# Kernel optimization log

Measured on AMD Instinct MI355X. Metric: run time of the kernel, lower is better.

## Reference

```python
import jax, jax.numpy as jnp
import numpy as np

B, C, T, COLS = 256, 1, 128, 512
IN_DIM = C * COLS          # 512
EMB = 1024
HID = 1024
NUM_LAYERS = 2
NUM_CLASSES = 10


def setup_inputs() -> dict:
    key = jax.random.key(0)
    ks = jax.random.split(key, 16)
    s = 0.05
    inp = {
        "x": jax.random.normal(ks[0], (B, C, T, COLS), dtype=jnp.float32),
        "W_enc": jax.random.normal(ks[1], (EMB, IN_DIM), dtype=jnp.float32) * s,
        "b_enc": jnp.zeros((EMB,), dtype=jnp.float32),
        # layer 0: input size EMB
        "W_ih0": jax.random.normal(ks[2], (4 * HID, EMB), dtype=jnp.float32) * s,
        "W_hh0": jax.random.normal(ks[3], (4 * HID, HID), dtype=jnp.float32) * s,
        "b_ih0": jnp.zeros((4 * HID,), dtype=jnp.float32),
        "b_hh0": jnp.zeros((4 * HID,), dtype=jnp.float32),
        # layer 1: input size HID
        "W_ih1": jax.random.normal(ks[4], (4 * HID, HID), dtype=jnp.float32) * s,
        "W_hh1": jax.random.normal(ks[5], (4 * HID, HID), dtype=jnp.float32) * s,
        "b_ih1": jnp.zeros((4 * HID,), dtype=jnp.float32),
        "b_hh1": jnp.zeros((4 * HID,), dtype=jnp.float32),
        "W_cls": jax.random.normal(ks[6], (NUM_CLASSES, HID), dtype=jnp.float32) * s,
        "b_cls": jnp.zeros((NUM_CLASSES,), dtype=jnp.float32),
    }
    return inp


def _lstm_cell(x, h, c, W_ih, W_hh, b_ih, b_hh):
    # gates: [B, 4H], PyTorch gate order i, f, g, o
    gates = x @ W_ih.T + b_ih + h @ W_hh.T + b_hh
    i, f, g, o = jnp.split(gates, 4, axis=-1)
    i = jax.nn.sigmoid(i)
    f = jax.nn.sigmoid(f)
    g = jnp.tanh(g)
    o = jax.nn.sigmoid(o)
    c_new = f * c + i * g
    h_new = o * jnp.tanh(c_new)
    return h_new, c_new


def reference(x, W_enc, b_enc, W_ih0, W_hh0, b_ih0, b_hh0,
              W_ih1, W_hh1, b_ih1, b_hh1, W_cls, b_cls):
    b_size = x.shape[0]
    # [B, C, T, COLS] -> [B, T, C*COLS]
    x_rowed = x.reshape(b_size, T, IN_DIM)
    emb = x_rowed @ W_enc.T + b_enc            # [B, T, EMB]
    emb_t = jnp.transpose(emb, (1, 0, 2))      # [T, B, EMB]

    layer_params = [(W_ih0, W_hh0, b_ih0, b_hh0), (W_ih1, W_hh1, b_ih1, b_hh1)]
    h0 = jnp.zeros((NUM_LAYERS, b_size, HID), dtype=x.dtype)
    c0 = jnp.zeros((NUM_LAYERS, b_size, HID), dtype=x.dtype)

    def step(carry, x_t):
        h, c = carry  # each [L, B, H]
        inp = x_t
        hs, cs = [], []
        for l in range(NUM_LAYERS):
            h_l, c_l = _lstm_cell(inp, h[l], c[l], *layer_params[l])
            hs.append(h_l)
            cs.append(c_l)
            inp = h_l
        return (jnp.stack(hs), jnp.stack(cs)), inp

    (_, _), outs = jax.lax.scan(step, (h0, c0), emb_t)  # outs: [T, B, H]
    last = outs[-1]                                     # [B, H]
    y = last @ W_cls.T + b_cls                          # [B, 10]
    return y
```

## Files before the change

### kernel.cpp

```cpp
#include <hip/hip_runtime.h>

#define B_SZ   256
#define T_SZ   128
#define IN_DIM 512
#define EMB    1024
#define HID    1024
#define G4     4096
#define NCLS   10
#define PSTR   2560
#define NBLK   256

typedef __attribute__((ext_vector_type(8))) short short8v;
typedef __attribute__((ext_vector_type(4))) float floatx4;

__device__ __forceinline__ unsigned short bf16hi(float f) {
    union { float f; unsigned u; } v; v.f = f;
    unsigned r = v.u + 0x7fff + ((v.u >> 16) & 1);
    return (unsigned short)(r >> 16);
}
__device__ __forceinline__ float bf2f(unsigned short b) {
    union { unsigned u; float f; } v; v.u = ((unsigned)b) << 16;
    return v.f;
}

template<int BM,int BN,int BK,int TM,int TN>
__global__ __launch_bounds__((BM/TM)*(BN/TN))
void gemm_f32_nn(const float* __restrict__ A, const float* __restrict__ Bm,
                 float* __restrict__ C, int M, int N, int K) {
    constexpr int THREADS = (BM/TM)*(BN/TN);
    __shared__ float As[BK][BM+4];
    __shared__ float Bs[BK][BN+4];
    const int tid  = threadIdx.x;
    const int tcol = tid % (BN/TN);
    const int trow = tid / (BN/TN);
    const int bm   = blockIdx.y * BM;
    const int bn   = blockIdx.x * BN;
    float acc[TM][TN];
#pragma unroll
    for (int i = 0; i < TM; ++i)
#pragma unroll
        for (int j = 0; j < TN; ++j) acc[i][j] = 0.f;
    for (int k0 = 0; k0 < K; k0 += BK) {
#pragma unroll
        for (int r = 0; r < BM*BK/4; r += THREADS) {
            int i  = r + tid;
            int m  = i / (BK/4);
            int kk = (i % (BK/4)) * 4;
            const float4 v = *(const float4*)(&A[(size_t)(bm+m)*K + k0 + kk]);
            As[kk+0][m]=v.x; As[kk+1][m]=v.y; As[kk+2][m]=v.z; As[kk+3][m]=v.w;
        }
#pragma unroll
        for (int r = 0; r < BK*BN/4; r += THREADS) {
            int i  = r + tid;
            int kk = i / (BN/4);
            int n4 = (i % (BN/4)) * 4;
            const float4 v = *(const float4*)(&Bm[(size_t)(k0+kk)*N + bn + n4]);
            *(float4*)(&Bs[kk][n4]) = v;
        }
        __syncthreads();
#pragma unroll
        for (int k = 0; k < BK; ++k) {
            float a[TM], b[TN];
#pragma unroll
            for (int i = 0; i < TM; ++i) a[i] = As[k][trow*TM+i];
#pragma unroll
            for (int j = 0; j < TN; ++j) b[j] = Bs[k][tcol*TN+j];
#pragma unroll
            for (int i = 0; i < TM; ++i)
#pragma unroll
                for (int j = 0; j < TN; ++j) acc[i][j] += a[i]*b[j];
        }
        __syncthreads();
    }
#pragma unroll
    for (int i = 0; i < TM; ++i)
#pragma unroll
        for (int j = 0; j < TN; ++j)
            C[(size_t)(bm+trow*TM+i)*N + bn + tcol*TN + j] = acc[i][j];
}

__global__ void swz2(const float* __restrict__ M0, int K0, int kf0,
                     const float* __restrict__ M1, int K1, int kfcnt,
                     unsigned short* __restrict__ dst) {
    int gid = blockIdx.x * 256 + threadIdx.x;
    int l   = gid & 63;
    int kf  = (gid >> 6) % kfcnt;
    int cf  = gid / (64 * kfcnt);
    int n   = cf*16 + (l & 15);
    int row = ((n & 3) << 10) + (n >> 2);
    const float* src; int kk = (l >> 4) * 8;
    if (kf < kf0) { src = M0 + (size_t)row * K0; kk += kf * 32; }
    else          { src = M1 + (size_t)row * K1; kk += (kf - kf0) * 32; }
    short8v vh, vl;
#pragma unroll
    for (int j = 0; j < 8; ++j) {
        float f = src[kk + j];
        unsigned short h = bf16hi(f);
        vh[j] = (short)h;
        vl[j] = (short)bf16hi(f - bf2f(h));
    }
    size_t base = ((size_t)(cf * kfcnt + kf) * 2) * 512 + (size_t)l * 8;
    *(short8v*)(dst + base)       = vh;
    *(short8v*)(dst + base + 512) = vl;
}

__global__ void build_bcombI(const float* __restrict__ W_ih0, const float* __restrict__ b_enc,
                             const float* __restrict__ b_ih0, const float* __restrict__ b_hh0,
                             float* __restrict__ bcombI) {
    int row  = blockIdx.x * 4 + (threadIdx.x >> 6);
    int lane = threadIdx.x & 63;
    const float* w = W_ih0 + (size_t)row * EMB;
    float s = 0.f;
    for (int k = lane; k < EMB; k += 64) s += w[k] * b_enc[k];
#pragma unroll
    for (int o = 32; o > 0; o >>= 1) s += __shfl_down(s, o);
    if (lane == 0) {
        int n = ((row & 1023) << 2) | (row >> 10);
        bcombI[n] = s + b_ih0[row] + b_hh0[row];
    }
}

__global__ void addvI(const float* __restrict__ a, const float* __restrict__ b,
                      float* __restrict__ o) {
    int i = blockIdx.x * 256 + threadIdx.x;
    int n = ((i & 1023) << 2) | (i >> 10);
    o[n] = a[i] + b[i];
}

__device__ __forceinline__ void gridbar(unsigned* bar, unsigned target, int tid) {
    __syncthreads();
    if (tid == 0) {
        __threadfence();
        atomicAdd(bar, 1u);
        while (__hip_atomic_load(bar, __ATOMIC_RELAXED, __HIP_MEMORY_SCOPE_AGENT) < target)
            __builtin_amdgcn_s_sleep(1);
        __threadfence();
    }
    __syncthreads();
}

__device__ __forceinline__ void load_b(const unsigned short* bp0, const unsigned short* bp1, int kf,
                                       short8v& h0, short8v& l0, short8v& h1, short8v& l1) {
    const unsigned short* p0 = bp0 + (size_t)kf * 1024;
    const unsigned short* p1 = bp1 + (size_t)kf * 1024;
    h0 = *(const short8v*)p0; l0 = *(const short8v*)(p0 + 512);
    h1 = *(const short8v*)p1; l1 = *(const short8v*)(p1 + 512);
}

__device__ __forceinline__ void mfma24(const unsigned short (*A)[2][64][8], int rowhalf, int l,
                                       short8v bh0, short8v bl0, short8v bh1, short8v bl1,
                                       floatx4 (&acc)[4][2]) {
    short8v ah[4], al[4];
#pragma unroll
    for (int m = 0; m < 4; ++m) {
        ah[m] = *(const short8v*)&A[rowhalf*4 + m][0][l][0];
        al[m] = *(const short8v*)&A[rowhalf*4 + m][1][l][0];
    }
#pragma unroll
    for (int m = 0; m < 4; ++m) {
        acc[m][0] = __builtin_amdgcn_mfma_f32_16x16x32_bf16(ah[m], bh0, acc[m][0], 0, 0, 0);
        acc[m][0] = __builtin_amdgcn_mfma_f32_16x16x32_bf16(ah[m], bl0, acc[m][0], 0, 0, 0);
        acc[m][0] = __builtin_amdgcn_mfma_f32_16x16x32_bf16(al[m], bh0, acc[m][0], 0, 0, 0);
        acc[m][1] = __builtin_amdgcn_mfma_f32_16x16x32_bf16(ah[m], bh1, acc[m][1], 0, 0, 0);
        acc[m][1] = __builtin_amdgcn_mfma_f32_16x16x32_bf16(ah[m], bl1, acc[m][1], 0, 0, 0);
        acc[m][1] = __builtin_amdgcn_mfma_f32_16x16x32_bf16(al[m], bh1, acc[m][1], 0, 0, 0);
    }
}

__device__ __forceinline__ void store_xz(unsigned short* ph, unsigned short* pl,
                                         int bid, int tid, float2 xv) {
    unsigned short h0 = bf16hi(xv.x), h1 = bf16hi(xv.y);
    ushort2 hh; hh.x = h0; hh.y = h1;
    ushort2 lv; lv.x = bf16hi(xv.x - bf2f(h0)); lv.y = bf16hi(xv.y - bf2f(h1));
    size_t o = (size_t)bid * PSTR + tid * 2;
    *(ushort2*)(ph + o) = hh;
    *(ushort2*)(pl + o) = lv;
}

typedef unsigned short AslT[2][8][2][64][8];

__global__ __launch_bounds__(512, 1)
void lstm_persist(const float* __restrict__ x,
                  const unsigned short* __restrict__ WLz,
                  const unsigned short* __restrict__ WRz,
                  const float* __restrict__ biasLI, const float* __restrict__ biasRI,
                  unsigned short* __restrict__ p0h, unsigned short* __restrict__ p0l,
                  unsigned short* __restrict__ p1h, unsigned short* __restrict__ p1l,
                  const float* __restrict__ Wcls, const float* __restrict__ bcls,
                  float* __restrict__ out, unsigned* __restrict__ bar) {
    __shared__ unsigned char smem[65536];
    AslT*  Asl   = (AslT*)smem;
    float (*gtile)[68] = (float (*)[68])smem;

    const int tid = threadIdx.x, bid = blockIdx.x;
    const int w = tid >> 6, l = tid & 63;
    const int kgrp = w >> 2, sub = w & 3;
    const int rowhalf = sub & 1, colhalf = sub >> 1;
    const int cg = bid & 127, rg = bid >> 7;
    const bool is_left = (cg < 64);
    const int cgl = is_left ? cg : cg - 64;
    const int SMAX = is_left ? 24 : 32;
    const int kfcnt = 2 * SMAX;
    const int acol0 = is_left ? 0 : 512;
    const int hcol0 = is_left ? 512 : 1536;
    const int r0 = rg * 128;
    const unsigned short* Bz = is_left ? WLz : WRz;
    const float* biasI = is_left ? biasLI : biasRI;

    const int cf0 = cgl*4 + colhalf*2;
    const unsigned short* bp0 = Bz + ((size_t)cf0     * kfcnt) * 1024 + (size_t)l * 8;
    const unsigned short* bp1 = Bz + ((size_t)(cf0+1) * kfcnt) * 1024 + (size_t)l * 8;
    const int kbase = kgrp * SMAX;

    float bias0 = 0.f, bias1 = 0.f;
    if (kgrp == 0) {
        int cA = cgl*64 + colhalf*32 + (l & 15);
        bias0 = biasI[cA]; bias1 = biasI[cA + 16];
    }

    unsigned short* PH[2] = {p0h, p1h};
    unsigned short* PL[2] = {p0l, p1l};

    float cst[4];
#pragma unroll
    for (int i = 0; i < 4; ++i) cst[i] = 0.f;

    unsigned target = 0;

    if (tid < 256) {
        float2 xv = *(const float2*)&x[((size_t)bid * T_SZ) * IN_DIM + tid * 2];
        store_xz(p0h, p0l, bid, tid, xv);
    }
    target += NBLK; gridbar(bar, target, tid);

    for (int t = 0; t <= T_SZ; ++t) {
        const int cur = t & 1, nxt = cur ^ 1;
        const bool conv = (t < T_SZ - 1) && (tid < 256);
        float2 xv;
        if (conv) xv = *(const float2*)&x[((size_t)bid * T_SZ + t + 1) * IN_DIM + tid * 2];

        const bool active = is_left ? (t < T_SZ) : (t >= 1);
        if (active) {
            const unsigned short* ph  = PH[cur];
            const unsigned short* plo = PL[cur];

            floatx4 acc[4][2];
#pragma unroll
            for (int m = 0; m < 4; ++m) {
                acc[m][0] = (floatx4){bias0, bias0, bias0, bias0};
                acc[m][1] = (floatx4){bias1, bias1, bias1, bias1};
            }

            short8v sreg[4];
            auto stage_load = [&](int s1) {
#pragma unroll
                for (int i = 0; i < 4; ++i) {
                    int seg = w*4 + i;
                    int g = seg >> 4, mf = (seg >> 1) & 7, pl = seg & 1;
                    const unsigned short* p = pl ? plo : ph;
                    size_t o = (size_t)(r0 + mf*16 + (l & 15)) * PSTR
                             + acol0 + (g*SMAX + s1)*32 + ((l >> 4) * 8);
                    sreg[i] = *(const short8v*)(p + o);
                }
            };
            auto stage_write = [&](int b) {
#pragma unroll
                for (int i = 0; i < 4; ++i) {
                    int seg = w*4 + i;
                    int g = seg >> 4, mf = (seg >> 1) & 7, pl = seg & 1;
                    *(short8v*)&Asl[g][b][mf][pl][l][0] = sreg[i];
                }
            };

            short8v bAh0,bAl0,bAh1,bAl1, bBh0,bBl0,bBh1,bBl1;

            stage_load(0); stage_write(0);
            load_b(bp0, bp1, kbase + 0, bAh0, bAl0, bAh1, bAl1);
            load_b(bp0, bp1, kbase + 1, bBh0, bBl0, bBh1, bBl1);
            stage_load(1);
            __syncthreads();

            for (int s2 = 0; s2 < SMAX; s2 += 2) {
                if (s2 + 1 < SMAX) stage_write(1);
                if (s2 + 2 < SMAX) stage_load(s2 + 2);
                mfma24((const unsigned short (*)[2][64][8])Asl[kgrp][0],
                       rowhalf, l, bAh0, bAl0, bAh1, bAl1, acc);
                if (s2 + 2 < SMAX) load_b(bp0, bp1, kbase + s2 + 2, bAh0, bAl0, bAh1, bAl1);
                __syncthreads();
                if (s2 + 2 < SMAX) stage_write(0);
                if (s2 + 3 < SMAX) stage_load(s2 + 3);
                if (s2 + 1 < SMAX)
                    mfma24((const unsigned short (*)[2][64][8])Asl[kgrp][1],
                           rowhalf, l, bBh0, bBl0, bBh1, bBl1, acc);
                if (s2 + 3 < SMAX) load_b(bp0, bp1, kbase + s2 + 3, bBh0, bBl0, bBh1, bBl1);
                __syncthreads();
            }

            if (kgrp == 0) {
#pragma unroll
                for (int m = 0; m < 4; ++m)
#pragma unroll
                    for (int c = 0; c < 2; ++c) {
                        int col = colhalf*32 + c*16 + (l & 15);
#pragma unroll
                        for (int jj = 0; jj < 4; ++jj)
                            gtile[rowhalf*64 + m*16 + ((l >> 4)*4) + jj][col] = acc[m][c][jj];
                    }
            }
            __syncthreads();
            if (kgrp == 1) {
#pragma unroll
                for (int m = 0; m < 4; ++m)
#pragma unroll
                    for (int c = 0; c < 2; ++c) {
                        int col = colhalf*32 + c*16 + (l & 15);
#pragma unroll
                        for (int jj = 0; jj < 4; ++jj)
                            gtile[rowhalf*64 + m*16 + ((l >> 4)*4) + jj][col] += acc[m][c][jj];
                    }
            }
            __syncthreads();

            {
                int u = tid & 15, rq = tid >> 4;
                unsigned short* nh = PH[nxt];
                unsigned short* nl = PL[nxt];
#pragma unroll
                for (int i = 0; i < 4; ++i) {
                    int r = rq*4 + i;
                    float4 gq = *(const float4*)&gtile[r][4*u];
                    float ii = 1.f / (1.f + expf(-gq.x));
                    float ff = 1.f / (1.f + expf(-gq.y));
                    float gg = tanhf(gq.z);
                    float oo = 1.f / (1.f + expf(-gq.w));
                    float cn = ff * cst[i] + ii * gg;
                    cst[i] = cn;
                    float h = oo * tanhf(cn);
                    unsigned short hh = bf16hi(h);
                    size_t o = (size_t)(r0 + r) * PSTR + hcol0 + cgl*16 + u;
                    nh[o] = hh;
                    nl[o] = bf16hi(h - bf2f(hh));
                }
            }
        }

        if (conv) store_xz(PH[nxt], PL[nxt], bid, tid, xv);
        target += NBLK; gridbar(bar, target, tid);
    }

    {
        const unsigned short* hh = PH[(T_SZ + 1) & 1];
        const unsigned short* hl = PL[(T_SZ + 1) & 1];
        float part[NCLS];
#pragma unroll
        for (int n = 0; n < NCLS; ++n) part[n] = 0.f;
        for (int k = tid; k < HID; k += 512) {
            size_t o = (size_t)bid * PSTR + 1536 + k;
            float hv = bf2f(hh[o]) + bf2f(hl[o]);
#pragma unroll
            for (int n = 0; n < NCLS; ++n) part[n] += hv * Wcls[(size_t)n * HID + k];
        }
        float* red = (float*)smem;
        for (int n = 0; n < NCLS; ++n) {
            red[tid] = part[n];
            __syncthreads();
            for (int s = 256; s > 0; s >>= 1) {
                if (tid < s) red[tid] += red[tid + s];
                __syncthreads();
            }
            if (tid == 0) out[(size_t)bid * NCLS + n] = red[0] + bcls[n];
            __syncthreads();
        }
    }
}

extern "C" void kernel_launch(void* const* d_in, const int* in_sizes, int n_in,
                              void* d_out, int out_size, void* d_ws, size_t ws_size,
                              hipStream_t stream) {
    const float* x      = (const float*)d_in[0];
    const float* W_enc  = (const float*)d_in[1];
    const float* b_enc  = (const float*)d_in[2];
    const float* W_ih0  = (const float*)d_in[3];
    const float* W_hh0  = (const float*)d_in[4];
    const float* b_ih0  = (const float*)d_in[5];
    const float* b_hh0  = (const float*)d_in[6];
    const float* W_ih1  = (const float*)d_in[7];
    const float* W_hh1  = (const float*)d_in[8];
    const float* b_ih1  = (const float*)d_in[9];
    const float* b_hh1  = (const float*)d_in[10];
    const float* W_cls  = (const float*)d_in[11];
    const float* b_cls  = (const float*)d_in[12];
    float* out = (float*)d_out;

    float* ws = (float*)d_ws;
    size_t off = 0;
    unsigned short* WLz    = (unsigned short*)(ws + off); off += (size_t)G4 * 1536 * 2 / 2;
    unsigned short* WRz    = (unsigned short*)(ws + off); off += (size_t)G4 * 2048 * 2 / 2;
    float*          Wcomb  = ws + off;                    off += (size_t)G4 * IN_DIM;
    float*          biasLI = ws + off;                    off += G4;
    float*          biasRI = ws + off;                    off += G4;
    unsigned short* planes = (unsigned short*)(ws + off); off += (size_t)4 * B_SZ * PSTR / 2;
    unsigned*       bar    = (unsigned*)(ws + off);       off += 64;

    unsigned short* p0h = planes;
    unsigned short* p0l = p0h + (size_t)B_SZ * PSTR;
    unsigned short* p1h = p0l + (size_t)B_SZ * PSTR;
    unsigned short* p1l = p1h + (size_t)B_SZ * PSTR;

    gemm_f32_nn<128,128,16,8,8><<<dim3(IN_DIM/128, G4/128), 256, 0, stream>>>(
        W_ih0, W_enc, Wcomb, G4, IN_DIM, EMB);
    build_bcombI<<<G4/4, 256, 0, stream>>>(W_ih0, b_enc, b_ih0, b_hh0, biasLI);
    addvI<<<G4/256, 256, 0, stream>>>(b_ih1, b_hh1, biasRI);
    swz2<<<64*48, 256, 0, stream>>>(Wcomb, IN_DIM, 16, W_hh0, HID, 48, WLz);
    swz2<<<64*64, 256, 0, stream>>>(W_ih1, HID, 32, W_hh1, HID, 64, WRz);
    hipMemsetAsync(planes, 0, (size_t)4 * B_SZ * PSTR * 2, stream);
    hipMemsetAsync(bar, 0, sizeof(unsigned), stream);

    lstm_persist<<<NBLK, 512, 0, stream>>>(
        x, WLz, WRz, biasLI, biasRI,
        p0h, p0l, p1h, p1l, W_cls, b_cls, out, bar);
}
```

Before: 8.384 ms.

## Load A fragments directly to registers, drop LDS staging, remap blocks

The per-step GEMM no longer stages A (hidden-state hi/lo) tiles through shared memory with syncthreads between stages. Each wave now loads its A fragments straight from global memory into registers in a double-buffered slice, alongside the B weights. Block-to-(column group, row group) mapping is permuted, and launch bounds allow two blocks per CU with smaller LDS. The aim is to remove LDS round-trips and intra-step barriers, at the cost of redundant global/L2 reads of A across waves and higher register pressure.

New measurement: 11.02 ms. 31.4% more time.

```diff
diff --git a/kernel.cpp b/kernel.cpp
--- a/kernel.cpp
+++ b/kernel.cpp
@@ -139,34 +139,6 @@
     __syncthreads();
 }
 
-__device__ __forceinline__ void load_b(const unsigned short* bp0, const unsigned short* bp1, int kf,
-                                       short8v& h0, short8v& l0, short8v& h1, short8v& l1) {
-    const unsigned short* p0 = bp0 + (size_t)kf * 1024;
-    const unsigned short* p1 = bp1 + (size_t)kf * 1024;
-    h0 = *(const short8v*)p0; l0 = *(const short8v*)(p0 + 512);
-    h1 = *(const short8v*)p1; l1 = *(const short8v*)(p1 + 512);
-}
-
-__device__ __forceinline__ void mfma24(const unsigned short (*A)[2][64][8], int rowhalf, int l,
-                                       short8v bh0, short8v bl0, short8v bh1, short8v bl1,
-                                       floatx4 (&acc)[4][2]) {
-    short8v ah[4], al[4];
-#pragma unroll
-    for (int m = 0; m < 4; ++m) {
-        ah[m] = *(const short8v*)&A[rowhalf*4 + m][0][l][0];
-        al[m] = *(const short8v*)&A[rowhalf*4 + m][1][l][0];
-    }
-#pragma unroll
-    for (int m = 0; m < 4; ++m) {
-        acc[m][0] = __builtin_amdgcn_mfma_f32_16x16x32_bf16(ah[m], bh0, acc[m][0], 0, 0, 0);
-        acc[m][0] = __builtin_amdgcn_mfma_f32_16x16x32_bf16(ah[m], bl0, acc[m][0], 0, 0, 0);
-        acc[m][0] = __builtin_amdgcn_mfma_f32_16x16x32_bf16(al[m], bh0, acc[m][0], 0, 0, 0);
-        acc[m][1] = __builtin_amdgcn_mfma_f32_16x16x32_bf16(ah[m], bh1, acc[m][1], 0, 0, 0);
-        acc[m][1] = __builtin_amdgcn_mfma_f32_16x16x32_bf16(ah[m], bl1, acc[m][1], 0, 0, 0);
-        acc[m][1] = __builtin_amdgcn_mfma_f32_16x16x32_bf16(al[m], bh1, acc[m][1], 0, 0, 0);
-    }
-}
-
 __device__ __forceinline__ void store_xz(unsigned short* ph, unsigned short* pl,
                                          int bid, int tid, float2 xv) {
     unsigned short h0 = bf16hi(xv.x), h1 = bf16hi(xv.y);
@@ -177,9 +149,12 @@
     *(ushort2*)(pl + o) = lv;
 }
 
-typedef unsigned short AslT[2][8][2][64][8];
-
-__global__ __launch_bounds__(512, 1)
+struct SliceRegs {
+    short8v ah[4], al[4];
+    short8v bh0, bl0, bh1, bl1;
+};
+
+__global__ __launch_bounds__(512, 2)
 void lstm_persist(const float* __restrict__ x,
                   const unsigned short* __restrict__ WLz,
                   const unsigned short* __restrict__ WRz,
@@ -188,15 +163,14 @@
                   unsigned short* __restrict__ p1h, unsigned short* __restrict__ p1l,
                   const float* __restrict__ Wcls, const float* __restrict__ bcls,
                   float* __restrict__ out, unsigned* __restrict__ bar) {
-    __shared__ unsigned char smem[65536];
-    AslT*  Asl   = (AslT*)smem;
-    float (*gtile)[68] = (float (*)[68])smem;
+    __shared__ float gtile[128][68];
 
     const int tid = threadIdx.x, bid = blockIdx.x;
     const int w = tid >> 6, l = tid & 63;
     const int kgrp = w >> 2, sub = w & 3;
     const int rowhalf = sub & 1, colhalf = sub >> 1;
-    const int cg = bid & 127, rg = bid >> 7;
+    const int cg = (bid & 7) * 16 + (bid >> 4);
+    const int rg = (bid >> 3) & 1;
     const bool is_left = (cg < 64);
     const int cgl = is_left ? cg : cg - 64;
     const int SMAX = is_left ? 24 : 32;
@@ -212,6 +186,9 @@
     const unsigned short* bp1 = Bz + ((size_t)(cf0+1) * kfcnt) * 1024 + (size_t)l * 8;
     const int kbase = kgrp * SMAX;
 
+    const int arow = r0 + rowhalf*64 + (l & 15);
+    const int akol = (l >> 4) * 8;
+
     float bias0 = 0.f, bias1 = 0.f;
     if (kgrp == 0) {
         int cA = cgl*64 + colhalf*32 + (l & 15);
@@ -244,6 +221,21 @@
             const unsigned short* ph  = PH[cur];
             const unsigned short* plo = PL[cur];
 
+            auto load_slice = [&](int s, SliceRegs& S) {
+                const int kf = kbase + s;
+                const size_t ko = (size_t)acol0 + (size_t)kf * 32 + akol;
+#pragma unroll
+                for (int m = 0; m < 4; ++m) {
+                    size_t o = (size_t)(arow + m*16) * PSTR + ko;
+                    S.ah[m] = *(const short8v*)(ph + o);
+                    S.al[m] = *(const short8v*)(plo + o);
+                }
+                const unsigned short* p0 = bp0 + (size_t)kf * 1024;
+                const unsigned short* p1 = bp1 + (size_t)kf * 1024;
+                S.bh0 = *(const short8v*)p0; S.bl0 = *(const short8v*)(p0 + 512);
+                S.bh1 = *(const short8v*)p1; S.bl1 = *(const short8v*)(p1 + 512);
+            };
+
             floatx4 acc[4][2];
 #pragma unroll
             for (int m = 0; m < 4; ++m) {
@@ -251,51 +243,29 @@
                 acc[m][1] = (floatx4){bias1, bias1, bias1, bias1};
             }
 
-            short8v sreg[4];
-            auto stage_load = [&](int s1) {
-#pragma unroll
-                for (int i = 0; i < 4; ++i) {
-                    int seg = w*4 + i;
-                    int g = seg >> 4, mf = (seg >> 1) & 7, pl = seg & 1;
-                    const unsigned short* p = pl ? plo : ph;
-                    size_t o = (size_t)(r0 + mf*16 + (l & 15)) * PSTR
-                             + acol0 + (g*SMAX + s1)*32 + ((l >> 4) * 8);
-                    sreg[i] = *(const short8v*)(p + o);
+            auto do_mfma = [&](SliceRegs& S) {
+#pragma unroll
+                for (int m = 0; m < 4; ++m) {
+                    acc[m][0] = __builtin_amdgcn_mfma_f32_16x16x32_bf16(S.ah[m], S.bh0, acc[m][0], 0, 0, 0);
+                    acc[m][0] = __builtin_amdgcn_mfma_f32_16x16x32_bf16(S.ah[m], S.bl0, acc[m][0], 0, 0, 0);
+                    acc[m][0] = __builtin_amdgcn_mfma_f32_16x16x32_bf16(S.al[m], S.bh0, acc[m][0], 0, 0, 0);
+                    acc[m][1] = __builtin_amdgcn_mfma_f32_16x16x32_bf16(S.ah[m], S.bh1, acc[m][1], 0, 0, 0);
+                    acc[m][1] = __builtin_amdgcn_mfma_f32_16x16x32_bf16(S.ah[m], S.bl1, acc[m][1], 0, 0, 0);
+                    acc[m][1] = __builtin_amdgcn_mfma_f32_16x16x32_bf16(S.al[m], S.bh1, acc[m][1], 0, 0, 0);
                 }
             };
-            auto stage_write = [&](int b) {
-#pragma unroll
-                for (int i = 0; i < 4; ++i) {
-                    int seg = w*4 + i;
-                    int g = seg >> 4, mf = (seg >> 1) & 7, pl = seg & 1;
-                    *(short8v*)&Asl[g][b][mf][pl][l][0] = sreg[i];
-                }
-            };
-
-            short8v bAh0,bAl0,bAh1,bAl1, bBh0,bBl0,bBh1,bBl1;
-
-            stage_load(0); stage_write(0);
-            load_b(bp0, bp1, kbase + 0, bAh0, bAl0, bAh1, bAl1);
-            load_b(bp0, bp1, kbase + 1, bBh0, bBl0, bBh1, bBl1);
-            stage_load(1);
-            __syncthreads();
-
+
+            SliceRegs SA, SB;
+            load_slice(0, SA);
+            load_slice(1, SB);
             for (int s2 = 0; s2 < SMAX; s2 += 2) {
-                if (s2 + 1 < SMAX) stage_write(1);
-                if (s2 + 2 < SMAX) stage_load(s2 + 2);
-                mfma24((const unsigned short (*)[2][64][8])Asl[kgrp][0],
-                       rowhalf, l, bAh0, bAl0, bAh1, bAl1, acc);
-                if (s2 + 2 < SMAX) load_b(bp0, bp1, kbase + s2 + 2, bAh0, bAl0, bAh1, bAl1);
-                __syncthreads();
-                if (s2 + 2 < SMAX) stage_write(0);
-                if (s2 + 3 < SMAX) stage_load(s2 + 3);
-                if (s2 + 1 < SMAX)
-                    mfma24((const unsigned short (*)[2][64][8])Asl[kgrp][1],
-                           rowhalf, l, bBh0, bBl0, bBh1, bBl1, acc);
-                if (s2 + 3 < SMAX) load_b(bp0, bp1, kbase + s2 + 3, bBh0, bBl0, bBh1, bBl1);
-                __syncthreads();
-            }
-
+                do_mfma(SA);
+                if (s2 + 2 < SMAX) load_slice(s2 + 2, SA);
+                do_mfma(SB);
+                if (s2 + 3 < SMAX) load_slice(s2 + 3, SB);
+            }
+
+            __syncthreads();
             if (kgrp == 0) {
 #pragma unroll
                 for (int m = 0; m < 4; ++m)
@@ -360,7 +330,7 @@
 #pragma unroll
             for (int n = 0; n < NCLS; ++n) part[n] += hv * Wcls[(size_t)n * HID + k];
         }
-        float* red = (float*)smem;
+        float* red = (float*)gtile;
         for (int n = 0; n < NCLS; ++n) {
             red[tid] = part[n];
             __syncthreads();
```
